# Performance work log

Measured on AMD Instinct MI355X. Metric: run time of the kernel, lower is better.

## Reference

```python
import jax, jax.numpy as jnp
import numpy as np
import math
from math import ceil

# --- static configuration (matches init_kwargs / input_specs) ---
T, H, W = 10, 45, 80            # native 720p latent video grid
NUM_WIN = (2, 5, 5)             # num_windows passed to make_720Pwindows_bysize
D_MODEL = 512
HEADS = 4
HEAD_DIM = 128
ROPE_DIMS = (32, 48, 48)        # 3D RoPE split of head_dim over (t, h, w)
THETA = 10000.0
TXT_LEN = 64
N_VID = T * H * W


def _make_windows():
    """Replicates make_720Pwindows_bysize slicing; returns gather/scatter index tables."""
    t, h, w = T, H, W
    rnt, rnh, rnw = NUM_WIN
    scale = math.sqrt(45 * 80 / (h * w))
    rh, rw = round(h * scale), round(w * scale)
    wh, ww = ceil(rh / rnh), ceil(rw / rnw)
    wt = ceil(min(t, 30) / rnt)
    nt, nh, nw = ceil(t / wt), ceil(h / wh), ceil(w / ww)
    lin = np.arange(t * h * w).reshape(t, h, w)
    wins = []
    for iw in range(nw):
        for ih in range(nh):
            for it in range(nt):
                ts = slice(it * wt, min((it + 1) * wt, t))
                hs = slice(ih * wh, min((ih + 1) * wh, h))
                ws = slice(iw * ww, min((iw + 1) * ww, w))
                blk = lin[ts, hs, ws].reshape(-1)
                if blk.size:
                    wins.append(blk)
    assert len({x.size for x in wins}) == 1, 'chosen dims give uniform windows'
    idx = np.stack(wins)                      # [n_win, win_size] gather index
    src = np.argsort(idx.reshape(-1))         # inverse permutation (un-window)
    return idx, src

WIN_IDX_NP, SRC_IDX_NP = _make_windows()
N_WIN, WIN_SIZE = WIN_IDX_NP.shape


def _rope_tables():
    """3D RoPE cos/sin per vid token: head_dim split over (t,h,w) axes, interleaved pairs."""
    tt = np.broadcast_to(np.arange(T)[:, None, None], (T, H, W)).reshape(-1)
    hh = np.broadcast_to(np.arange(H)[None, :, None], (T, H, W)).reshape(-1)
    ww = np.broadcast_to(np.arange(W)[None, None, :], (T, H, W)).reshape(-1)
    cos_l, sin_l = [], []
    for pos, d in zip((tt, hh, ww), ROPE_DIMS):
        inv = 1.0 / (THETA ** (np.arange(0, d, 2, dtype=np.float64) / d))
        ang = pos[:, None].astype(np.float64) * inv[None, :]
        ang = np.repeat(ang, 2, axis=-1)
        cos_l.append(np.cos(ang))
        sin_l.append(np.sin(ang))
    cos = np.concatenate(cos_l, -1).astype(np.float32)
    sin = np.concatenate(sin_l, -1).astype(np.float32)
    return jnp.asarray(cos), jnp.asarray(sin)  # each [N_VID, HEAD_DIM]

ROPE_COS, ROPE_SIN = _rope_tables()


def _rotate_half(x):
    # '... (d r) -> ... d r' with r=2, then (-x2, x1) re-interleaved
    xr = x.reshape(x.shape[:-1] + (-1, 2))
    x1, x2 = xr[..., 0], xr[..., 1]
    return jnp.stack((-x2, x1), axis=-1).reshape(x.shape)


def _apply_rope(x, cos, sin):
    # x: [N, heads, D]; cos/sin: [N, D]
    return x * cos[:, None, :] + _rotate_half(x) * sin[:, None, :]


def setup_inputs() -> dict:
    key = jax.random.key(0)
    ks = jax.random.split(key, 6)
    s = 1.0 / math.sqrt(D_MODEL)
    return {
        'vid': jax.random.normal(ks[0], (N_VID, D_MODEL), jnp.float32),
        'txt': jax.random.normal(ks[1], (TXT_LEN, D_MODEL), jnp.float32),
        'w_qkv_vid': jax.random.normal(ks[2], (D_MODEL, 3 * D_MODEL), jnp.float32) * s,
        'w_qkv_txt': jax.random.normal(ks[3], (D_MODEL, 3 * D_MODEL), jnp.float32) * s,
        'w_out_vid': jax.random.normal(ks[4], (D_MODEL, D_MODEL), jnp.float32) * s,
        'w_out_txt': jax.random.normal(ks[5], (D_MODEL, D_MODEL), jnp.float32) * s,
    }


def reference(vid, txt, w_qkv_vid, w_qkv_txt, w_out_vid, w_out_txt):
    win_idx = jnp.asarray(WIN_IDX_NP)
    src_idx = jnp.asarray(SRC_IDX_NP)
    # per-modality QKV projection (MMModule: separate vid/txt weights)
    qkv_v = (vid @ w_qkv_vid).reshape(N_VID, 3, HEADS, HEAD_DIM)
    qv, kv, vv = qkv_v[:, 0], qkv_v[:, 1], qkv_v[:, 2]
    qv = _apply_rope(qv, ROPE_COS, ROPE_SIN)   # 3D RoPE on video q/k only
    kv = _apply_rope(kv, ROPE_COS, ROPE_SIN)
    qkv_t = (txt @ w_qkv_txt).reshape(TXT_LEN, 3, HEADS, HEAD_DIM)
    qt, kt, vt = qkv_t[:, 0], qkv_t[:, 1], qkv_t[:, 2]

    def win_cat(xv, xt):
        xw = xv[win_idx]
        xtb = jnp.broadcast_to(xt[None], (N_WIN,) + xt.shape)    # txt repeated per window
        return jnp.concatenate([xw, xtb], axis=1)                # [n_win, S, H, D]

    q, k, v = win_cat(qv, qt), win_cat(kv, kt), win_cat(vv, vt)
    scale = 1.0 / math.sqrt(HEAD_DIM)
    scores = jnp.einsum('wqhd,wkhd->whqk', q, k) * scale         # [n_win, H, S, S]
    probs = jax.nn.softmax(scores, axis=-1)
    out = jnp.einsum('whqk,wkhd->wqhd', probs, v)                # [n_win, S, H, D]
    # un-window vid tokens (inverse permutation), mean-coalesce txt over windows
    out_v = out[:, :WIN_SIZE].reshape(N_WIN * WIN_SIZE, D_MODEL)[src_idx]
    out_t = out[:, WIN_SIZE:].mean(axis=0).reshape(TXT_LEN, D_MODEL)
    return jnp.concatenate([out_v @ w_out_vid, out_t @ w_out_txt], axis=0)
```

## Files before the change

kernel.cpp:

```cpp
#include <hip/hip_runtime.h>
#include <hip/hip_bf16.h>


typedef unsigned short u16;
typedef unsigned int   u32;
typedef float v4f __attribute__((ext_vector_type(4)));
typedef short v8s __attribute__((ext_vector_type(8)));

#define N_VID    36000
#define MPAD     36096
#define DM       512
#define NW       50
#define WSZ      720
#define SEQ      784
#define SP       832
#define QK_SCALE_L2E 0.12751743f
#define L2THETA  13.287712379549449f

union U8 { uint4 u; u16 s[8]; };

__device__ __forceinline__ u16 f2b(float f) {
  u32 u = __builtin_bit_cast(u32, f);
  u32 r = (u + 0x7FFFu + ((u >> 16) & 1u)) >> 16;
  return (u16)r;
}
__device__ __forceinline__ float b2f(u16 h) {
  u32 u = ((u32)h) << 16;
  return __builtin_bit_cast(float, u);
}
__device__ __forceinline__ u32 pkhi(float lo, float hi) {
  return __builtin_amdgcn_perm(__builtin_bit_cast(u32, hi),
                               __builtin_bit_cast(u32, lo), 0x07060302u);
}
__device__ __forceinline__ int vperm4(int l0) {
  return (l0 & ~31) + (((l0 & 15) >> 2) << 3) + (((l0 >> 4) & 1) << 2);
}

__device__ __forceinline__ void gload_lds16(const void* g, void* l) {
  __builtin_amdgcn_global_load_lds(
      (const __attribute__((address_space(1))) void*)g,
      (__attribute__((address_space(3))) void*)l,
      16, 0, 0);
}

__global__ __launch_bounds__(256) void k_prep(const float* __restrict__ vid,
                                              const float* __restrict__ txt,
                                              u16* __restrict__ vid_b,
                                              u16* __restrict__ txt_b,
                                              const float* __restrict__ wqv,
                                              const float* __restrict__ wqt,
                                              const float* __restrict__ wov,
                                              u16* __restrict__ o0,
                                              u16* __restrict__ o1,
                                              u16* __restrict__ o2) {
  __shared__ u16 lt[64 * 72];
  int t = threadIdx.x;
  if (blockIdx.x < 9088) {
    int id  = blockIdx.x * 256 + t;
    int row = id >> 6, oct = id & 63;
    U8 o;
    if (row < MPAD) {
      if (row < N_VID) {
        const float* s = vid + (size_t)row * DM + oct * 8;
        float4 a = *(const float4*)s, b = *(const float4*)(s + 4);
        o.s[0]=f2b(a.x); o.s[1]=f2b(a.y); o.s[2]=f2b(a.z); o.s[3]=f2b(a.w);
        o.s[4]=f2b(b.x); o.s[5]=f2b(b.y); o.s[6]=f2b(b.z); o.s[7]=f2b(b.w);
      } else { o.u = make_uint4(0,0,0,0); }
      *(uint4*)&vid_b[(size_t)row * DM + oct * 8] = o.u;
    } else {
      int tr = row - MPAD;
      if (tr >= 256) return;
      if (tr < 64) {
        const float* s = txt + (size_t)tr * DM + oct * 8;
        float4 a = *(const float4*)s, b = *(const float4*)(s + 4);
        o.s[0]=f2b(a.x); o.s[1]=f2b(a.y); o.s[2]=f2b(a.z); o.s[3]=f2b(a.w);
        o.s[4]=f2b(b.x); o.s[5]=f2b(b.y); o.s[6]=f2b(b.z); o.s[7]=f2b(b.w);
      } else { o.u = make_uint4(0,0,0,0); }
      *(uint4*)&txt_b[(size_t)tr * DM + oct * 8] = o.u;
    }
    return;
  }
  int b = blockIdx.x - 9088;
  const float* src; u16* dst; int N; int tb;
  if (b < 192)      { src = wqv; dst = o0; N = 1536; tb = b; }
  else if (b < 384) { src = wqt; dst = o1; N = 1536; tb = b - 192; }
  else              { src = wov; dst = o2; N = 512;  tb = b - 384; }
  int kt = tb & 7, nt = tb >> 3;
  int k0 = kt * 64, n0 = nt * 64;
#pragma unroll
  for (int pass = 0; pass < 16; ++pass) {
    int kl = pass * 4 + (t >> 6), nl = t & 63;
    float v = src[(size_t)(k0 + kl) * N + n0 + nl];
    lt[nl * 72 + kl] = f2b(v);
  }
  __syncthreads();
#pragma unroll
  for (int pass = 0; pass < 2; ++pass) {
    int slot = pass * 256 + t;
    int nr = slot >> 3, ko = slot & 7;
    U8 o;
#pragma unroll
    for (int j = 0; j < 8; ++j) o.s[j] = lt[nr * 72 + ko * 8 + j];
    *(uint4*)&dst[(size_t)(n0 + nr) * 512 + k0 + ko * 8] = o.u;
  }
}

template <int F32OUT>
__device__ __forceinline__ void gemm_body(const u16* __restrict__ A,
                                          const u16* __restrict__ Bt,
                                          void* __restrict__ Cout,
                                          int N, int K, int Mstore,
                                          int m0, int n0) {
  __shared__ u16 lA[128 * 32];
  __shared__ u16 lB[128 * 32];
  int t = threadIdx.x, wv = t >> 6, L = t & 63;
  int wm = wv & 1, wn = wv >> 1;
  v4f acc[4][4] = {};
  const int kiters = K >> 5;
  const u16* ga = A + (size_t)(m0 + wv * 32 + (L >> 2)) * K + (L & 3) * 8;
  const u16* gb = Bt + (size_t)(n0 + wv * 32 + (L >> 2)) * K + (L & 3) * 8;
  u16* la = lA + (wv * 32) * 32;
  u16* lb = lB + (wv * 32) * 32;
  for (int kt = 0; kt < kiters; ++kt) {
    __syncthreads();
    gload_lds16(ga,                 la);
    gload_lds16(ga + (size_t)16 * K, la + 16 * 32);
    gload_lds16(gb,                 lb);
    gload_lds16(gb + (size_t)16 * K, lb + 16 * 32);
    ga += 32; gb += 32;
    __syncthreads();
    v8s af[4], bf[4];
#pragma unroll
    for (int i = 0; i < 4; ++i) {
      af[i] = *(const v8s*)&lA[(wm * 64 + i * 16 + (L & 15)) * 32 + (L >> 4) * 8];
      bf[i] = *(const v8s*)&lB[(wn * 64 + i * 16 + (L & 15)) * 32 + (L >> 4) * 8];
    }
#pragma unroll
    for (int i = 0; i < 4; ++i)
#pragma unroll
      for (int j = 0; j < 4; ++j)
        acc[i][j] = __builtin_amdgcn_mfma_f32_16x16x32_bf16(af[i], bf[j], acc[i][j], 0, 0, 0);
  }
#pragma unroll
  for (int i = 0; i < 4; ++i) {
#pragma unroll
    for (int r = 0; r < 4; ++r) {
      int row = m0 + wm * 64 + i * 16 + (L >> 4) * 4 + r;
      if (row < Mstore) {
#pragma unroll
        for (int j = 0; j < 4; ++j) {
          int col = n0 + wn * 64 + j * 16 + (L & 15);
          if (F32OUT) ((float*)Cout)[(size_t)row * N + col] = acc[i][j][r];
          else        ((u16*)Cout)[(size_t)row * N + col] = f2b(acc[i][j][r]);
        }
      }
    }
  }
}

__global__ __launch_bounds__(512, 2) void k_gemm_qkv(const u16* __restrict__ A,
                                                     const u16* __restrict__ Bt,
                                                     u16* __restrict__ Cv,
                                                     const u16* __restrict__ At,
                                                     const u16* __restrict__ Btt,
                                                     u16* __restrict__ Ct) {
  __shared__ u16 lA[2][256 * 64];
  __shared__ u16 lB[2][256 * 64];
  int t = threadIdx.x, wv = t >> 6, L = t & 63;
  int wm = wv >> 2, wn = wv & 3;
  int colL = L & 15, quad = L >> 4;
  int mt = blockIdx.x, nt = blockIdx.y;
  const u16* Ap; const u16* Bp; u16* Cp; int m0; bool mask;
  if (mt < 141) { Ap = A;  Bp = Bt;  Cp = Cv; m0 = mt * 256; mask = false; }
  else          { Ap = At; Bp = Btt; Cp = Ct; m0 = 0;        mask = true;  }
  int n0 = nt * 256;

  int srow = wv * 32 + (L >> 3);
  int sblk = (L & 7) ^ (L >> 3);
  const u16* gA = Ap + (size_t)(m0 + srow) * 512 + sblk * 8;
  const u16* gB = Bp + (size_t)(n0 + srow) * 512 + sblk * 8;

  auto stage = [&](int kt, int buf) {
#pragma unroll
    for (int c = 0; c < 4; ++c) {
      gload_lds16(gA + (size_t)c * 8 * 512 + kt * 64,
                  &lA[buf][(wv * 32 + c * 8) * 64]);
      gload_lds16(gB + (size_t)c * 8 * 512 + kt * 64,
                  &lB[buf][(wv * 32 + c * 8) * 64]);
    }
  };

  v4f acc[8][4] = {};
  int ra = (wm * 128 + colL) * 64;
  int rb = (wn * 64 + colL) * 64;
  int x0 = ((quad) ^ (colL & 7)) * 8;
  int x1 = ((4 + quad) ^ (colL & 7)) * 8;

  stage(0, 0);
  stage(1, 1);
  asm volatile("s_waitcnt vmcnt(8)" ::: "memory");
  __builtin_amdgcn_s_barrier();

  for (int kt = 0; kt < 8; ++kt) {
    int buf = kt & 1;
    const u16* pa = &lA[buf][0];
    const u16* pb = &lB[buf][0];
    {
      v8s af[8], bf[4];
#pragma unroll
      for (int fm = 0; fm < 8; ++fm) af[fm] = *(const v8s*)&pa[ra + fm * 1024 + x0];
#pragma unroll
      for (int fn = 0; fn < 4; ++fn) bf[fn] = *(const v8s*)&pb[rb + fn * 1024 + x0];
      __builtin_amdgcn_s_setprio(1);
#pragma unroll
      for (int fm = 0; fm < 8; ++fm)
#pragma unroll
        for (int fn = 0; fn < 4; ++fn)
          acc[fm][fn] = __builtin_amdgcn_mfma_f32_16x16x32_bf16(af[fm], bf[fn], acc[fm][fn], 0, 0, 0);
      __builtin_amdgcn_s_setprio(0);
    }
    {
      v8s af[8], bf[4];
#pragma unroll
      for (int fm = 0; fm < 8; ++fm) af[fm] = *(const v8s*)&pa[ra + fm * 1024 + x1];
#pragma unroll
      for (int fn = 0; fn < 4; ++fn) bf[fn] = *(const v8s*)&pb[rb + fn * 1024 + x1];
      __builtin_amdgcn_s_setprio(1);
#pragma unroll
      for (int fm = 0; fm < 8; ++fm)
#pragma unroll
        for (int fn = 0; fn < 4; ++fn)
          acc[fm][fn] = __builtin_amdgcn_mfma_f32_16x16x32_bf16(af[fm], bf[fn], acc[fm][fn], 0, 0, 0);
      __builtin_amdgcn_s_setprio(0);
    }
    if (kt < 7) {
      __builtin_amdgcn_s_barrier();
      if (kt + 2 < 8) {
        stage(kt + 2, buf);
        asm volatile("s_waitcnt vmcnt(8)" ::: "memory");
      } else {
        asm volatile("s_waitcnt vmcnt(0)" ::: "memory");
      }
      __builtin_amdgcn_s_barrier();
    }
  }

#pragma unroll
  for (int fm = 0; fm < 8; ++fm) {
#pragma unroll
    for (int r = 0; r < 4; ++r) {
      int row = m0 + wm * 128 + fm * 16 + quad * 4 + r;
      if (!mask || row < 128) {
#pragma unroll
        for (int fn = 0; fn < 4; ++fn) {
          int col = n0 + wn * 64 + fn * 16 + colL;
          Cp[(size_t)row * 1536 + col] = f2b(acc[fm][fn][r]);
        }
      }
    }
  }
}

__global__ __launch_bounds__(256) void k_ropegather(const u16* __restrict__ qkv,
                                                    const u16* __restrict__ qkvt,
                                                    u16* __restrict__ Q,
                                                    u16* __restrict__ K,
                                                    u16* __restrict__ Vt) {
  __shared__ u16 lv[512 * 18];
  int t = threadIdx.x;
  int w = blockIdx.y;
  if (blockIdx.x >= 45) {
    int tb = (blockIdx.x - 45) * 256 + t;
#pragma unroll
    for (int k = 0; k < 4; ++k) {
      int o = tb * 4 + k;
      int h = o >> 10, p64 = (o >> 4) & 63, c8 = o & 15;
      U8 q, kk;
      q.u  = *(const uint4*)&qkvt[(size_t)p64 * 1536 + h * 128 + c8 * 8];
      kk.u = *(const uint4*)&qkvt[(size_t)p64 * 1536 + 512 + h * 128 + c8 * 8];
#pragma unroll
      for (int j = 0; j < 8; ++j) q.s[j] = f2b(b2f(q.s[j]) * QK_SCALE_L2E);
      size_t base = (((size_t)w * 4 + h) * SP + WSZ + p64) * 128 + c8 * 8;
      *(uint4*)&Q[base] = q.u;
      *(uint4*)&K[base] = kk.u;
    }
#pragma unroll
    for (int k = 0; k < 8; ++k) {
      int vr = tb * 8 + k;
      int h = vr >> 11, ch = (vr >> 4) & 127, run = vr & 15;
      int l0 = WSZ + run * 4;
      uint2 o;
      u16* os = (u16*)&o;
#pragma unroll
      for (int j = 0; j < 4; ++j)
        os[j] = qkvt[(size_t)(l0 - WSZ + j) * 1536 + 1024 + h * 128 + ch];
      *(uint2*)&Vt[(((size_t)w * 4 + h) * 128 + ch) * SP + vperm4(l0)] = o;
    }
    return;
  }
  int pt = blockIdx.x;
  int p_local = t >> 4;
  int p = pt * 16 + p_local;
  int iw = w / 10; int r10 = w - iw * 10; int ih = r10 >> 1; int it = r10 & 1;
  int dt = p / 144; int rem = p - dt * 144; int dh = rem >> 4; int dw = rem & 15;
  int tt = it * 5 + dt, hh = ih * 9 + dh, wx = iw * 16 + dw;
  int n = tt * 3600 + hh * 80 + wx;
  const size_t qrow = (size_t)n * 1536;
#pragma unroll
  for (int it2 = 0; it2 < 12; ++it2) {
    int oct = it2 * 16 + (t & 15);
    int col = oct * 8;
    U8 x; x.u = *(const uint4*)&qkv[qrow + col];
    if (col < 1024) {
      int cc = col & 511; int h = cc >> 7; int ch = cc & 127;
      int pos, i0; float dinv;
      if (ch < 32)      { pos = tt; i0 = ch >> 1;        dinv = 1.f / 32.f; }
      else if (ch < 80) { pos = hh; i0 = (ch - 32) >> 1; dinv = 1.f / 48.f; }
      else              { pos = wx; i0 = (ch - 80) >> 1; dinv = 1.f / 48.f; }
      bool isQ = col < 512;
      float sc = isQ ? QK_SCALE_L2E : 1.0f;
      U8 o;
#pragma unroll
      for (int pr = 0; pr < 4; ++pr) {
        float inv = exp2f(-2.f * (float)(i0 + pr) * dinv * L2THETA);
        float ang = (float)pos * inv;
        float s, c; __sincosf(ang, &s, &c);
        float x0 = b2f(x.s[2 * pr]), x1 = b2f(x.s[2 * pr + 1]);
        o.s[2 * pr]     = f2b((x0 * c - x1 * s) * sc);
        o.s[2 * pr + 1] = f2b((x1 * c + x0 * s) * sc);
      }
      u16* dst = isQ ? Q : K;
      *(uint4*)&dst[(((size_t)w * 4 + h) * SP + p) * 128 + ch] = o.u;
    } else {
      int cv = col - 1024;
#pragma unroll
      for (int j = 0; j < 8; ++j) lv[(cv + j) * 18 + p_local] = x.s[j];
    }
  }
  __syncthreads();
#pragma unroll
  for (int it3 = 0; it3 < 4; ++it3) {
    int slot = it3 * 256 + t; int cv = slot >> 1; int half = slot & 1;
    U8 o;
#pragma unroll
    for (int j = 0; j < 8; ++j) o.s[j] = lv[cv * 18 + half * 8 + j];
    int h = cv >> 7, ch = cv & 127;
    int P0 = pt * 16 + half * 8;
    size_t base = (((size_t)w * 4 + h) * 128 + ch) * SP;
    *(uint2*)&Vt[base + vperm4(P0)]     = make_uint2(o.u.x, o.u.y);
    *(uint2*)&Vt[base + vperm4(P0 + 4)] = make_uint2(o.u.z, o.u.w);
  }
}

__global__ __launch_bounds__(256) void k_attn(const u16* __restrict__ Q,
                                              const u16* __restrict__ Kb,
                                              const u16* __restrict__ Vt,
                                              u16* __restrict__ outr,
                                              float* __restrict__ txt_acc) {
  __shared__ u16 lK[2][4 * 64 * 32];
  __shared__ u16 lV[2][2 * 128 * 32];
  int t = threadIdx.x, wv = t >> 6, L = t & 63;
  int id = blockIdx.x;
  int xcd = id & 7, sidx = id >> 3;
  int whg = sidx / 7;  int qt = sidx - whg * 7;
  int wh = whg * 8 + xcd;
  int w = wh >> 2, h = wh & 3;
  size_t whq = ((size_t)wh) * SP * 128;
  int q0 = qt * 128 + wv * 32;
  bool live = q0 < SEQ;
  if (q0 > 800) q0 = 800;
  int colL = L & 15, quad = L >> 4;
  v8s qf[2][4];
#pragma unroll
  for (int s = 0; s < 2; ++s) {
    const u16* qp = Q + whq + (size_t)(q0 + s * 16 + colL) * 128 + quad * 8;
#pragma unroll
    for (int kc = 0; kc < 4; ++kc) qf[s][kc] = *(const v8s*)(qp + kc * 32);
  }
  float li[2] = {0.f, 0.f};
  v4f O[2][8] = {};

  auto stage = [&](int kt, int buf) {
#pragma unroll
    for (int pass = 0; pass < 4; ++pass) {
      int cr = wv * 64 + pass * 16 + (L >> 2);
      int kc = cr >> 6, row = cr & 63;
      gload_lds16(Kb + whq + (size_t)(kt * 64 + row) * 128 + kc * 32 + (L & 3) * 8,
                  (u16*)&lK[buf][0] + (size_t)(wv * 64 + pass * 16) * 32);
      int kc2 = cr >> 7, ch = cr & 127;
      gload_lds16(Vt + whq + (size_t)ch * SP + kt * 64 + kc2 * 32 + (L & 3) * 8,
                  (u16*)&lV[buf][0] + (size_t)(wv * 64 + pass * 16) * 32);
    }
  };

  stage(0, 0);
  __syncthreads();

  for (int kt = 0; kt < 13; ++kt) {
    int cur = kt & 1;
    if (kt < 12) stage(kt + 1, cur ^ 1);

    if (live) {
      const u16* lKc = &lK[cur][0];
      const u16* lVc = &lV[cur][0];

      v4f ST[2][4] = {};
      __builtin_amdgcn_s_setprio(1);
#pragma unroll
      for (int kc = 0; kc < 4; ++kc) {
#pragma unroll
        for (int nbk = 0; nbk < 4; ++nbk) {
          v8s kf = *(const v8s*)&lKc[(kc * 64 + nbk * 16 + colL) * 32 + quad * 8];
          ST[0][nbk] = __builtin_amdgcn_mfma_f32_16x16x32_bf16(kf, qf[0][kc], ST[0][nbk], 0, 0, 0);
          ST[1][nbk] = __builtin_amdgcn_mfma_f32_16x16x32_bf16(kf, qf[1][kc], ST[1][nbk], 0, 0, 0);
        }
      }
      __builtin_amdgcn_s_setprio(0);

      union { v8s v; u32 wd[4]; } Bf[2][2];
#pragma unroll
      for (int s = 0; s < 2; ++s) {
#pragma unroll
        for (int nbk = 0; nbk < 4; ++nbk) {
          float ev[4];
          if (kt * 64 + nbk * 16 < SEQ) {
#pragma unroll
            for (int r = 0; r < 4; ++r) {
              float e = __builtin_amdgcn_exp2f(ST[s][nbk][r]);
              u32 tb = __builtin_bit_cast(u32, e) & 0xFFFF0000u;
              float tf = __builtin_bit_cast(float, tb);
              li[s] += tf;
              ev[r] = tf;
            }
          } else {
#pragma unroll
            for (int r = 0; r < 4; ++r) ev[r] = 0.f;
          }
          Bf[nbk >> 1][s].wd[(nbk & 1) * 2 + 0] = pkhi(ev[0], ev[1]);
          Bf[nbk >> 1][s].wd[(nbk & 1) * 2 + 1] = pkhi(ev[2], ev[3]);
        }
      }

      __builtin_amdgcn_s_setprio(1);
#pragma unroll
      for (int kc2 = 0; kc2 < 2; ++kc2) {
#pragma unroll
        for (int nbo = 0; nbo < 8; ++nbo) {
          v8s af = *(const v8s*)&lVc[(kc2 * 128 + nbo * 16 + colL) * 32 + quad * 8];
          O[0][nbo] = __builtin_amdgcn_mfma_f32_16x16x32_bf16(af, Bf[kc2][0].v, O[0][nbo], 0, 0, 0);
          O[1][nbo] = __builtin_amdgcn_mfma_f32_16x16x32_bf16(af, Bf[kc2][1].v, O[1][nbo], 0, 0, 0);
        }
      }
      __builtin_amdgcn_s_setprio(0);
    }

    __syncthreads();
  }

  if (!live) return;

  float linv[2];
#pragma unroll
  for (int s = 0; s < 2; ++s) {
    float v = li[s];
    v += __shfl_xor(v, 16);
    v += __shfl_xor(v, 32);
    linv[s] = 1.f / v;
  }

  int iw = w / 10; int r10 = w - iw * 10; int ih = r10 >> 1; int it = r10 & 1;
#pragma unroll
  for (int s = 0; s < 2; ++s) {
    int p = q0 + s * 16 + colL;
    if (p < WSZ) {
      int dt = p / 144; int rem = p - dt * 144; int dh = rem >> 4; int dw = rem & 15;
      int n = (it * 5 + dt) * 3600 + (ih * 9 + dh) * 80 + iw * 16 + dw;
      size_t rowbase = (size_t)n * DM + h * 128 + quad * 4;
#pragma unroll
      for (int nbo = 0; nbo < 8; ++nbo) {
        uint2 st;
        st.x = (u32)f2b(O[s][nbo][0] * linv[s]) | ((u32)f2b(O[s][nbo][1] * linv[s]) << 16);
        st.y = (u32)f2b(O[s][nbo][2] * linv[s]) | ((u32)f2b(O[s][nbo][3] * linv[s]) << 16);
        *(uint2*)&outr[rowbase + nbo * 16] = st;
      }
    } else if (p < SEQ) {
      size_t rb = (size_t)(p - WSZ) * DM + h * 128 + quad * 4;
#pragma unroll
      for (int nbo = 0; nbo < 8; ++nbo)
#pragma unroll
        for (int r = 0; r < 4; ++r)
          atomicAdd(&txt_acc[rb + nbo * 16 + r], O[s][nbo][r] * linv[s] * 0.02f);
    }
  }
}

__global__ __launch_bounds__(256) void k_gemm_out(const u16* __restrict__ A,
                                                  const u16* __restrict__ Bt,
                                                  float* __restrict__ out,
                                                  const float* __restrict__ acc,
                                                  const float* __restrict__ wo) {
  if (blockIdx.x < 282) {
    gemm_body<1>(A, Bt, out, 512, 512, N_VID, blockIdx.x * 128, blockIdx.y * 128);
    return;
  }
  int r = (blockIdx.x - 282) * 4 + blockIdx.y;
  int t = threadIdx.x;
  float s0 = 0.f, s1 = 0.f;
  for (int k = 0; k < 512; ++k) {
    float a = acc[r * 512 + k];
    s0 = fmaf(a, wo[k * 512 + t], s0);
    s1 = fmaf(a, wo[k * 512 + t + 256], s1);
  }
  float* ob = out + (size_t)N_VID * DM;
  ob[(size_t)r * 512 + t] = s0;
  ob[(size_t)r * 512 + t + 256] = s1;
}

extern "C" void kernel_launch(void* const* d_in, const int* in_sizes, int n_in,
                              void* d_out, int out_size, void* d_ws, size_t ws_size,
                              hipStream_t stream) {
  const float* vid       = (const float*)d_in[0];
  const float* txt       = (const float*)d_in[1];
  const float* w_qkv_vid = (const float*)d_in[2];
  const float* w_qkv_txt = (const float*)d_in[3];
  const float* w_out_vid = (const float*)d_in[4];
  const float* w_out_txt = (const float*)d_in[5];
  float* out = (float*)d_out;
  char* ws = (char*)d_ws;

  size_t off = 0;
  u16* vid_b   = (u16*)(ws + off); off += (size_t)MPAD * DM * 2;
  u16* txt_b   = (u16*)(ws + off); off += 256 * DM * 2;
  u16* wt_qv   = (u16*)(ws + off); off += 1536 * 512 * 2;
  u16* wt_qt   = (u16*)(ws + off); off += 1536 * 512 * 2;
  u16* wt_ov   = (u16*)(ws + off); off += 512 * 512 * 2;
  u16* qkv_v   = (u16*)(ws + off); off += (size_t)MPAD * 1536 * 2;
  u16* qkv_t   = (u16*)(ws + off); off += 128 * 1536 * 2;
  u16* Qb      = (u16*)(ws + off); off += (size_t)NW * 4 * SP * 128 * 2;
  u16* Kb      = (u16*)(ws + off); off += (size_t)NW * 4 * SP * 128 * 2;
  u16* Vtb     = (u16*)(ws + off); off += (size_t)NW * 4 * 128 * SP * 2;
  float* tacc  = (float*)(ws + off); off += 64 * 512 * 4;
  u16* out_rows = vid_b;

  hipMemsetAsync(tacc, 0, 64 * 512 * 4, stream);

  k_prep<<<9536, 256, 0, stream>>>(vid, txt, vid_b, txt_b,
                                   w_qkv_vid, w_qkv_txt, w_out_vid,
                                   wt_qv, wt_qt, wt_ov);

  k_gemm_qkv<<<dim3(142, 6), 512, 0, stream>>>(vid_b, wt_qv, qkv_v,
                                               txt_b, wt_qt, qkv_t);

  k_ropegather<<<dim3(49, 50), 256, 0, stream>>>(qkv_v, qkv_t, Qb, Kb, Vtb);

  k_attn<<<1400, 256, 0, stream>>>(Qb, Kb, Vtb, out_rows, tacc);

  k_gemm_out<<<dim3(298, 4), 256, 0, stream>>>(out_rows, wt_ov, out, tacc, w_out_txt);
}
```

Before: 450.3 us.

## Software-pipeline attention loop: overlap next QK^T with current softmax·V

Restructures the flash-attention K-tile loop so the QK^T MFMAs for tile k+1 are issued together with the exp/softmax and PV MFMAs for tile k, using two score register sets (STa/STb) in ping-pong fashion. V staging moves to a triple-buffered LDS ring, since a V tile must survive one extra iteration, while K stays double-buffered. The goal is to hide exp/pack latency and LDS reads behind independent matrix work. The cost is more live registers, which may reduce occupancy or cause spills, plus extra LDS. The setprio hints are also dropped.

```diff
diff --git a/kernel.cpp b/kernel.cpp
--- a/kernel.cpp
+++ b/kernel.cpp
@@ -358,7 +358,7 @@
                                               u16* __restrict__ outr,
                                               float* __restrict__ txt_acc) {
   __shared__ u16 lK[2][4 * 64 * 32];
-  __shared__ u16 lV[2][2 * 128 * 32];
+  __shared__ u16 lV[3][2 * 128 * 32];
   int t = threadIdx.x, wv = t >> 6, L = t & 63;
   int id = blockIdx.x;
   int xcd = id & 7, sidx = id >> 3;
@@ -379,85 +379,91 @@
   }
   float li[2] = {0.f, 0.f};
   v4f O[2][8] = {};
-
-  auto stage = [&](int kt, int buf) {
+  v4f STa[2][4], STb[2][4];
+
+  auto stage = [&](int kt) {
+    int bK = kt & 1, bV = kt % 3;
 #pragma unroll
     for (int pass = 0; pass < 4; ++pass) {
       int cr = wv * 64 + pass * 16 + (L >> 2);
       int kc = cr >> 6, row = cr & 63;
       gload_lds16(Kb + whq + (size_t)(kt * 64 + row) * 128 + kc * 32 + (L & 3) * 8,
-                  (u16*)&lK[buf][0] + (size_t)(wv * 64 + pass * 16) * 32);
+                  (u16*)&lK[bK][0] + (size_t)(wv * 64 + pass * 16) * 32);
       int kc2 = cr >> 7, ch = cr & 127;
       gload_lds16(Vt + whq + (size_t)ch * SP + kt * 64 + kc2 * 32 + (L & 3) * 8,
-                  (u16*)&lV[buf][0] + (size_t)(wv * 64 + pass * 16) * 32);
+                  (u16*)&lV[bV][0] + (size_t)(wv * 64 + pass * 16) * 32);
     }
   };
 
-  stage(0, 0);
+  auto qk = [&](int kt, v4f (&ST)[2][4]) {
+    const u16* lKc = &lK[kt & 1][0];
+#pragma unroll
+    for (int s = 0; s < 2; ++s)
+#pragma unroll
+      for (int nbk = 0; nbk < 4; ++nbk) ST[s][nbk] = (v4f){0.f, 0.f, 0.f, 0.f};
+#pragma unroll
+    for (int kc = 0; kc < 4; ++kc) {
+#pragma unroll
+      for (int nbk = 0; nbk < 4; ++nbk) {
+        v8s kf = *(const v8s*)&lKc[(kc * 64 + nbk * 16 + colL) * 32 + quad * 8];
+        ST[0][nbk] = __builtin_amdgcn_mfma_f32_16x16x32_bf16(kf, qf[0][kc], ST[0][nbk], 0, 0, 0);
+        ST[1][nbk] = __builtin_amdgcn_mfma_f32_16x16x32_bf16(kf, qf[1][kc], ST[1][nbk], 0, 0, 0);
+      }
+    }
+  };
+
+  auto smpv = [&](int kt, v4f (&ST)[2][4]) {
+    const u16* lVc = &lV[kt % 3][0];
+    union { v8s v; u32 wd[4]; } Bf[2][2];
+#pragma unroll
+    for (int s = 0; s < 2; ++s) {
+#pragma unroll
+      for (int nbk = 0; nbk < 4; ++nbk) {
+        float ev[4];
+        if (kt * 64 + nbk * 16 < SEQ) {
+#pragma unroll
+          for (int r = 0; r < 4; ++r) {
+            float e = __builtin_amdgcn_exp2f(ST[s][nbk][r]);
+            u32 tb = __builtin_bit_cast(u32, e) & 0xFFFF0000u;
+            float tf = __builtin_bit_cast(float, tb);
+            li[s] += tf;
+            ev[r] = tf;
+          }
+        } else {
+#pragma unroll
+          for (int r = 0; r < 4; ++r) ev[r] = 0.f;
+        }
+        Bf[nbk >> 1][s].wd[(nbk & 1) * 2 + 0] = pkhi(ev[0], ev[1]);
+        Bf[nbk >> 1][s].wd[(nbk & 1) * 2 + 1] = pkhi(ev[2], ev[3]);
+      }
+    }
+#pragma unroll
+    for (int kc2 = 0; kc2 < 2; ++kc2) {
+#pragma unroll
+      for (int nbo = 0; nbo < 8; ++nbo) {
+        v8s af = *(const v8s*)&lVc[(kc2 * 128 + nbo * 16 + colL) * 32 + quad * 8];
+        O[0][nbo] = __builtin_amdgcn_mfma_f32_16x16x32_bf16(af, Bf[kc2][0].v, O[0][nbo], 0, 0, 0);
+        O[1][nbo] = __builtin_amdgcn_mfma_f32_16x16x32_bf16(af, Bf[kc2][1].v, O[1][nbo], 0, 0, 0);
+      }
+    }
+  };
+
+  stage(0);
   __syncthreads();
-
-  for (int kt = 0; kt < 13; ++kt) {
-    int cur = kt & 1;
-    if (kt < 12) stage(kt + 1, cur ^ 1);
-
-    if (live) {
-      const u16* lKc = &lK[cur][0];
-      const u16* lVc = &lV[cur][0];
-
-      v4f ST[2][4] = {};
-      __builtin_amdgcn_s_setprio(1);
-#pragma unroll
-      for (int kc = 0; kc < 4; ++kc) {
-#pragma unroll
-        for (int nbk = 0; nbk < 4; ++nbk) {
-          v8s kf = *(const v8s*)&lKc[(kc * 64 + nbk * 16 + colL) * 32 + quad * 8];
-          ST[0][nbk] = __builtin_amdgcn_mfma_f32_16x16x32_bf16(kf, qf[0][kc], ST[0][nbk], 0, 0, 0);
-          ST[1][nbk] = __builtin_amdgcn_mfma_f32_16x16x32_bf16(kf, qf[1][kc], ST[1][nbk], 0, 0, 0);
-        }
-      }
-      __builtin_amdgcn_s_setprio(0);
-
-      union { v8s v; u32 wd[4]; } Bf[2][2];
-#pragma unroll
-      for (int s = 0; s < 2; ++s) {
-#pragma unroll
-        for (int nbk = 0; nbk < 4; ++nbk) {
-          float ev[4];
-          if (kt * 64 + nbk * 16 < SEQ) {
-#pragma unroll
-            for (int r = 0; r < 4; ++r) {
-              float e = __builtin_amdgcn_exp2f(ST[s][nbk][r]);
-              u32 tb = __builtin_bit_cast(u32, e) & 0xFFFF0000u;
-              float tf = __builtin_bit_cast(float, tb);
-              li[s] += tf;
-              ev[r] = tf;
-            }
-          } else {
-#pragma unroll
-            for (int r = 0; r < 4; ++r) ev[r] = 0.f;
-          }
-          Bf[nbk >> 1][s].wd[(nbk & 1) * 2 + 0] = pkhi(ev[0], ev[1]);
-          Bf[nbk >> 1][s].wd[(nbk & 1) * 2 + 1] = pkhi(ev[2], ev[3]);
-        }
-      }
-
-      __builtin_amdgcn_s_setprio(1);
-#pragma unroll
-      for (int kc2 = 0; kc2 < 2; ++kc2) {
-#pragma unroll
-        for (int nbo = 0; nbo < 8; ++nbo) {
-          v8s af = *(const v8s*)&lVc[(kc2 * 128 + nbo * 16 + colL) * 32 + quad * 8];
-          O[0][nbo] = __builtin_amdgcn_mfma_f32_16x16x32_bf16(af, Bf[kc2][0].v, O[0][nbo], 0, 0, 0);
-          O[1][nbo] = __builtin_amdgcn_mfma_f32_16x16x32_bf16(af, Bf[kc2][1].v, O[1][nbo], 0, 0, 0);
-        }
-      }
-      __builtin_amdgcn_s_setprio(0);
-    }
-
+  stage(1);
+  if (live) qk(0, STa);
+  __syncthreads();
+
+  for (int k2 = 1; k2 < 13; k2 += 2) {
+    stage(k2 + 1);
+    if (live) { qk(k2, STb); smpv(k2 - 1, STa); }
     __syncthreads();
-  }
-
-  if (!live) return;
+    if (k2 + 2 < 13) stage(k2 + 2);
+    if (live) { qk(k2 + 1, STa); smpv(k2, STb); }
+    __syncthreads();
+  }
+  if (live) smpv(12, STa);
+  else return;
 
   float linv[2];
 #pragma unroll
```

Result: slower. 493.0 us (+9.5%).
